# Performance work log

Measured on AMD Instinct MI355X. Metric: run time of the kernel, lower is better.

Reference implementation:

```python
import jax, jax.numpy as jnp
import numpy as np


def _l2_normalize(x, eps=1e-12):
    # matches torch F.normalize(p=2): x / max(||x||, eps)
    n = jnp.linalg.norm(x, axis=-1, keepdims=True)
    return x / jnp.maximum(n, eps)


def _linear_sum_assignment(cost):
    """Jonker-Volgenant shortest augmenting path (same optimum as scipy
    linear_sum_assignment) for a square cost matrix. Returns col4row:
    col4row[r] = column assigned to row r (minimization)."""
    n = cost.shape[0]
    INF = np.inf
    u = np.zeros(n + 1)
    v = np.zeros(n + 1)
    p = np.zeros(n + 1, dtype=np.int64)   # p[j] = row (1-based) assigned to col j
    way = np.zeros(n + 1, dtype=np.int64)
    for i in range(1, n + 1):
        p[0] = i
        j0 = 0
        minv = np.full(n + 1, INF)
        used = np.zeros(n + 1, dtype=bool)
        while True:
            used[j0] = True
            i0 = p[j0]
            cur = cost[i0 - 1] - u[i0] - v[1:]          # reduced costs of row i0
            free = ~used[1:]
            upd = free & (cur < minv[1:])
            idx = np.nonzero(upd)[0]
            minv[idx + 1] = cur[idx]
            way[idx + 1] = j0
            freeidx = np.nonzero(free)[0]
            jrel = freeidx[np.argmin(minv[freeidx + 1])]
            delta = minv[jrel + 1]
            u[p[used]] += delta
            v[used] -= delta
            minv[~used] -= delta
            j0 = jrel + 1
            if p[j0] == 0:
                break
        while j0:
            j1 = way[j0]
            p[j0] = p[j1]
            j0 = j1
    col4row = np.empty(n, dtype=np.int64)
    col4row[p[1:] - 1] = np.arange(n)
    return col4row


def setup_inputs() -> dict:
    key = jax.random.key(0)
    k1, k2 = jax.random.split(key)
    B, N, D = 128, 256, 64
    inputs = jax.random.normal(k1, (B, N, D), dtype=jnp.float32)
    targets = jax.random.normal(k2, (B, N, D), dtype=jnp.float32)
    return {"inputs": inputs, "targets": targets}


def reference(inputs, targets):
    ip = _l2_normalize(inputs)                     # [B, N, D]
    tg = _l2_normalize(targets)                    # [B, N, D]
    cos = jnp.einsum('bad,bcd->bac', ip, tg)       # [B, N, N]
    self_cos = jnp.einsum('bad,bcd->bac', ip, ip)  # [B, N, N]
    # strip the diagonal: tril(-1)[:, :-1] + triu(1)[:, 1:] -> [B, N, N-1]
    self_off = jnp.tril(self_cos, k=-1)[:, :, :-1] + jnp.triu(self_cos, k=1)[:, :, 1:]
    # Hungarian assignment on host (non-differentiable, as in the torch code)
    cost = np.asarray(jax.lax.stop_gradient(-cos))
    tgt = jnp.asarray(np.stack([_linear_sum_assignment(cost[b]) for b in range(cost.shape[0])]))  # [B, N]
    logits = jnp.concatenate([cos, self_off], axis=-1)        # [B, N, 2N-1]
    logp = jax.nn.log_softmax(logits, axis=-1)
    nll = -jnp.take_along_axis(logp, tgt[..., None], axis=-1)[..., 0]  # [B, N]
    # per-sample cross_entropy is mean over N; batch_loss / B -> global mean
    return jnp.mean(nll)
```

## Files before the change

### kernel.cpp

```cpp
#include <hip/hip_runtime.h>
#include <hip/hip_fp16.h>
#include <math.h>

#define BB 128
#define NN 256
#define DD 64
constexpr int NROWS = BB * NN;

__global__ __launch_bounds__(256) void norm_kernel(const float* __restrict__ inp,
                                                   const float* __restrict__ tgin,
                                                   float* __restrict__ ipn,
                                                   float* __restrict__ tgn) {
  int wid = threadIdx.x >> 6;
  int lane = threadIdx.x & 63;
  int row = blockIdx.x * 4 + wid;
  const float* src;
  float* dst;
  int r = row;
  if (row < NROWS) { src = inp; dst = ipn; }
  else { src = tgin; dst = tgn; r = row - NROWS; }
  float x = src[(size_t)r * DD + lane];
  float s = x * x;
  #pragma unroll
  for (int off = 32; off; off >>= 1) s += __shfl_xor(s, off);
  float nrm = sqrtf(s);
  float scale = 1.0f / fmaxf(nrm, 1e-12f);
  dst[(size_t)r * DD + lane] = x * scale;
}

__global__ __launch_bounds__(256) void gemm_kernel(const float* __restrict__ ipn,
                                                   const float* __restrict__ tgn,
                                                   float* __restrict__ cosm,
                                                   float* __restrict__ selfm) {
  __shared__ float As[64 * 64];
  __shared__ float Bs[64 * 64];
  int b = blockIdx.y;
  int ti = (blockIdx.x >> 2) * 64;
  int tj = (blockIdx.x & 3) * 64;
  const float* A = ipn + (size_t)b * NN * DD + (size_t)ti * DD;
  const float* Bm = (blockIdx.z ? ipn : tgn) + (size_t)b * NN * DD + (size_t)tj * DD;
  float* Out = (blockIdx.z ? selfm : cosm) + (size_t)b * NN * NN;
  int t = threadIdx.x;
  #pragma unroll
  for (int i = 0; i < 4; ++i) {
    int f4 = t + 256 * i;
    int row = f4 >> 4;
    int k0 = (f4 & 15) << 2;
    float4 a = reinterpret_cast<const float4*>(A)[f4];
    float4 v = reinterpret_cast<const float4*>(Bm)[f4];
    As[(k0 + 0) * 64 + row] = a.x; As[(k0 + 1) * 64 + row] = a.y;
    As[(k0 + 2) * 64 + row] = a.z; As[(k0 + 3) * 64 + row] = a.w;
    Bs[(k0 + 0) * 64 + row] = v.x; Bs[(k0 + 1) * 64 + row] = v.y;
    Bs[(k0 + 2) * 64 + row] = v.z; Bs[(k0 + 3) * 64 + row] = v.w;
  }
  __syncthreads();
  int tx = t & 15, ty = t >> 4;
  float acc[4][4] = {};
  #pragma unroll 8
  for (int k = 0; k < 64; ++k) {
    float4 av = *reinterpret_cast<const float4*>(&As[k * 64 + ty * 4]);
    float4 bv = *reinterpret_cast<const float4*>(&Bs[k * 64 + tx * 4]);
    float ar[4] = {av.x, av.y, av.z, av.w};
    float br[4] = {bv.x, bv.y, bv.z, bv.w};
    #pragma unroll
    for (int r = 0; r < 4; ++r)
      #pragma unroll
      for (int c = 0; c < 4; ++c)
        acc[r][c] = fmaf(ar[r], br[c], acc[r][c]);
  }
  #pragma unroll
  for (int r = 0; r < 4; ++r) {
    float4 o = {acc[r][0], acc[r][1], acc[r][2], acc[r][3]};
    *reinterpret_cast<float4*>(&Out[(size_t)(ti + ty * 4 + r) * NN + tj + tx * 4]) = o;
  }
}

__device__ __forceinline__ int sel4i(const int a[4], int q) {
  int r = a[0];
  if (q == 1) r = a[1];
  else if (q == 2) r = a[2];
  else if (q == 3) r = a[3];
  return r;
}
__device__ __forceinline__ void set4i(int a[4], int q, int v) {
  if (q == 0) a[0] = v;
  else if (q == 1) a[1] = v;
  else if (q == 2) a[2] = v;
  else a[3] = v;
}
__device__ __forceinline__ int readlane_i(int x, int l) {
  return __builtin_amdgcn_readlane(x, l);
}
__device__ __forceinline__ float readlane_f(float x, int l) {
  return __builtin_bit_cast(float, __builtin_amdgcn_readlane(__builtin_bit_cast(int, x), l));
}
__device__ __forceinline__ float wave_min_f32(float x) {
  float t;
  #define DPP_STEP(ctrl)                                                            \
    t = __builtin_bit_cast(float, __builtin_amdgcn_update_dpp(                      \
            __builtin_bit_cast(int, x), __builtin_bit_cast(int, x), ctrl, 0xF, 0xF, \
            false));                                                                \
    x = fminf(x, t);
  DPP_STEP(0x111)
  DPP_STEP(0x112)
  DPP_STEP(0x114)
  DPP_STEP(0x118)
  DPP_STEP(0x142)
  DPP_STEP(0x143)
  #undef DPP_STEP
  return x;
}

__global__ __launch_bounds__(64) void hungarian_kernel(const float* __restrict__ cosm,
                                                       int* __restrict__ tgt) {
  const int b = blockIdx.x;
  const float* __restrict__ C = cosm + (size_t)b * NN * NN;
  __shared__ __half Cs[NN * NN];
  __shared__ float u_lds[NN];
  const int lane = threadIdx.x;
  const float FINF = INFINITY;

  const float4* Cf4 = reinterpret_cast<const float4*>(C);
  #pragma unroll 4
  for (int it = 0; it < NN * NN / 4 / 64; ++it) {
    float4 f = Cf4[it * 64 + lane];
    __half2 h01 = __floats2half2_rn(f.x, f.y);
    __half2 h23 = __floats2half2_rn(f.z, f.w);
    __half2* dst = reinterpret_cast<__half2*>(&Cs[(it * 64 + lane) * 4]);
    dst[0] = h01;
    dst[1] = h23;
  }
  #pragma unroll
  for (int q = 0; q < 4; ++q) u_lds[lane * 4 + q] = 0.f;

  float v[4] = {0.f, 0.f, 0.f, 0.f};
  int p[4] = {0, 0, 0, 0};

  for (int i = 1; i <= NN; ++i) {
    float minv[4] = {FINF, FINF, FINF, FINF};
    int way[4] = {-2, -2, -2, -2};
    int usedm = 0;
    float Delta = 0.f;
    int j0 = -1;
    float u_i0 = 0.f;
    int row = i - 1;
    uint2 raw = *reinterpret_cast<const uint2*>(&Cs[(size_t)row * NN + lane * 4]);
    int jf;

    while (true) {
      __half2 h01 = __builtin_bit_cast(__half2, raw.x);
      __half2 h23 = __builtin_bit_cast(__half2, raw.y);
      float2 f01 = __half22float2(h01);
      float2 f23 = __half22float2(h23);
      float cc[4] = {f01.x, f01.y, f23.x, f23.y};
      float t0 = Delta - u_i0;
      float cand[4];
      #pragma unroll
      for (int q = 0; q < 4; ++q) {
        float dnew = t0 - cc[q] - v[q];
        bool freeq = !((usedm >> q) & 1);
        if (freeq && dnew < minv[q]) { minv[q] = dnew; way[q] = j0; }
        cand[q] = freeq ? minv[q] : FINF;
      }
      float bv = cand[0];
      int bc = lane * 4;
      #pragma unroll
      for (int q = 1; q < 4; ++q)
        if (cand[q] < bv) { bv = cand[q]; bc = lane * 4 + q; }
      float m = wave_min_f32(bv);
      float K = readlane_f(m, 63);
      unsigned long long mask = __ballot(bv == K);
      int l0 = __ffsll(mask) - 1;
      int j1 = readlane_i(bc, l0);
      Delta = K;
      int pnext = readlane_i(sel4i(p, j1 & 3), j1 >> 2);
      if (pnext == 0) { jf = j1; break; }
      if (lane == (j1 >> 2)) usedm |= 1 << (j1 & 3);
      j0 = j1;
      row = pnext - 1;
      raw = *reinterpret_cast<const uint2*>(&Cs[(size_t)row * NN + lane * 4]);
      u_i0 = u_lds[row];
    }

    #pragma unroll
    for (int q = 0; q < 4; ++q) {
      if ((usedm >> q) & 1) {
        float dd = Delta - minv[q];
        v[q] -= dd;
        u_lds[p[q] - 1] += dd;
      }
    }
    if (lane == 0) u_lds[i - 1] = Delta;

    int j = jf;
    while (true) {
      int w = readlane_i(sel4i(way, j & 3), j >> 2);
      int newv;
      if (w < 0) newv = i;
      else newv = readlane_i(sel4i(p, w & 3), w >> 2);
      if (lane == (j >> 2)) set4i(p, j & 3, newv);
      if (w < 0) break;
      j = w;
    }
  }
  #pragma unroll
  for (int q = 0; q < 4; ++q)
    tgt[(size_t)b * NN + (p[q] - 1)] = lane * 4 + q;
}

__global__ __launch_bounds__(256) void nll_kernel(const float* __restrict__ cosm,
                                                  const float* __restrict__ selfm,
                                                  const int* __restrict__ tgt,
                                                  float* __restrict__ nll) {
  int lane = threadIdx.x & 63, wid = threadIdx.x >> 6;
  int row = blockIdx.x * 4 + wid;
  int r = row & (NN - 1);
  const float* crow = cosm + (size_t)row * NN;
  const float* srow = selfm + (size_t)row * NN;
  float xc[4], xs[4];
  float m = -INFINITY;
  #pragma unroll
  for (int q = 0; q < 4; ++q) {
    int j = lane + 64 * q;
    xc[q] = crow[j];
    xs[q] = (j == r) ? -INFINITY : srow[j];
    m = fmaxf(m, fmaxf(xc[q], xs[q]));
  }
  #pragma unroll
  for (int off = 32; off; off >>= 1) m = fmaxf(m, __shfl_xor(m, off));
  float s = 0.f;
  #pragma unroll
  for (int q = 0; q < 4; ++q) {
    s += expf(xc[q] - m);
    s += (xs[q] == -INFINITY) ? 0.f : expf(xs[q] - m);
  }
  #pragma unroll
  for (int off = 32; off; off >>= 1) s += __shfl_xor(s, off);
  if (lane == 0) {
    float lse = m + logf(s);
    nll[row] = lse - crow[tgt[row]];
  }
}

__global__ __launch_bounds__(256) void reduce_kernel(const float* __restrict__ nll,
                                                     float* __restrict__ out) {
  __shared__ float sm[256];
  int t = threadIdx.x;
  float s = 0.f;
  for (int i = t; i < NROWS; i += 256) s += nll[i];
  sm[t] = s;
  __syncthreads();
  for (int st = 128; st; st >>= 1) {
    if (t < st) sm[t] += sm[t + st];
    __syncthreads();
  }
  if (t == 0) out[0] = sm[0] / (float)NROWS;
}

extern "C" void kernel_launch(void* const* d_in, const int* in_sizes, int n_in,
                              void* d_out, int out_size, void* d_ws, size_t ws_size,
                              hipStream_t stream) {
  const float* inputs = (const float*)d_in[0];
  const float* targets = (const float*)d_in[1];
  float* ws = (float*)d_ws;
  float* ipn = ws;
  float* tgn = ipn + (size_t)BB * NN * DD;
  float* cosm = tgn + (size_t)BB * NN * DD;
  float* selfm = cosm + (size_t)BB * NN * NN;
  int* tgt = (int*)(selfm + (size_t)BB * NN * NN);
  float* nll = (float*)(tgt + BB * NN);

  norm_kernel<<<2 * NROWS / 4, 256, 0, stream>>>(inputs, targets, ipn, tgn);
  gemm_kernel<<<dim3(16, BB, 2), 256, 0, stream>>>(ipn, tgn, cosm, selfm);
  hungarian_kernel<<<BB, 64, 0, stream>>>(cosm, tgt);
  nll_kernel<<<NROWS / 4, 256, 0, stream>>>(cosm, selfm, tgt, nll);
  reduce_kernel<<<1, 256, 0, stream>>>(nll, (float*)d_out);
}
```

Measured before the change: 1.303 ms.

## Switch Hungarian solver to packed integer keys with fused column index

The Hungarian kernel now quantizes the cost into 16-bit fixed-point integers in LDS and runs the shortest-augmenting-path loop in integer arithmetic. The reduced distance and the column index are packed into one 32-bit key, so a single unsigned wave-min gives both the minimum and its argmin. This drops the ballot/ffs/readlane argmin sequence and the half-to-float conversions from the serial inner loop. The next row load is also issued earlier in the loop. In exchange the costs are quantized to about 1/32768, and ties between columns are broken by lowest index. The change assumes the packed key never overflows, so assignments on near-tied costs may differ from the float version.

```diff
diff --git a/kernel.cpp b/kernel.cpp
--- a/kernel.cpp
+++ b/kernel.cpp
@@ -1,5 +1,4 @@
 #include <hip/hip_runtime.h>
-#include <hip/hip_fp16.h>
 #include <math.h>
 
 #define BB 128
@@ -91,16 +90,12 @@
 __device__ __forceinline__ int readlane_i(int x, int l) {
   return __builtin_amdgcn_readlane(x, l);
 }
-__device__ __forceinline__ float readlane_f(float x, int l) {
-  return __builtin_bit_cast(float, __builtin_amdgcn_readlane(__builtin_bit_cast(int, x), l));
-}
-__device__ __forceinline__ float wave_min_f32(float x) {
-  float t;
-  #define DPP_STEP(ctrl)                                                            \
-    t = __builtin_bit_cast(float, __builtin_amdgcn_update_dpp(                      \
-            __builtin_bit_cast(int, x), __builtin_bit_cast(int, x), ctrl, 0xF, 0xF, \
-            false));                                                                \
-    x = fminf(x, t);
+__device__ __forceinline__ unsigned wave_min_u32(unsigned x) {
+  unsigned t;
+  #define DPP_STEP(ctrl)                                                        \
+    t = (unsigned)__builtin_amdgcn_update_dpp((int)x, (int)x, ctrl, 0xF, 0xF,   \
+                                              false);                           \
+    x = (t < x) ? t : x;
   DPP_STEP(0x111)
   DPP_STEP(0x112)
   DPP_STEP(0x114)
@@ -115,78 +110,83 @@
                                                        int* __restrict__ tgt) {
   const int b = blockIdx.x;
   const float* __restrict__ C = cosm + (size_t)b * NN * NN;
-  __shared__ __half Cs[NN * NN];
-  __shared__ float u_lds[NN];
+  __shared__ unsigned short Cs[NN * NN];
+  __shared__ int u_lds[NN];
   const int lane = threadIdx.x;
-  const float FINF = INFINITY;
+  const int col0 = lane * 4;
 
   const float4* Cf4 = reinterpret_cast<const float4*>(C);
   #pragma unroll 4
   for (int it = 0; it < NN * NN / 4 / 64; ++it) {
     float4 f = Cf4[it * 64 + lane];
-    __half2 h01 = __floats2half2_rn(f.x, f.y);
-    __half2 h23 = __floats2half2_rn(f.z, f.w);
-    __half2* dst = reinterpret_cast<__half2*>(&Cs[(it * 64 + lane) * 4]);
-    dst[0] = h01;
-    dst[1] = h23;
-  }
-  #pragma unroll
-  for (int q = 0; q < 4; ++q) u_lds[lane * 4 + q] = 0.f;
-
-  float v[4] = {0.f, 0.f, 0.f, 0.f};
+    unsigned u0 = __float2uint_rn(fmaxf(32768.f - f.x * 32768.f, 0.f));
+    unsigned u1 = __float2uint_rn(fmaxf(32768.f - f.y * 32768.f, 0.f));
+    unsigned u2 = __float2uint_rn(fmaxf(32768.f - f.z * 32768.f, 0.f));
+    unsigned u3 = __float2uint_rn(fmaxf(32768.f - f.w * 32768.f, 0.f));
+    u0 = u0 > 65535u ? 65535u : u0;
+    u1 = u1 > 65535u ? 65535u : u1;
+    u2 = u2 > 65535u ? 65535u : u2;
+    u3 = u3 > 65535u ? 65535u : u3;
+    uint2 packed;
+    packed.x = u0 | (u1 << 16);
+    packed.y = u2 | (u3 << 16);
+    *reinterpret_cast<uint2*>(&Cs[(it * 64 + lane) * 4]) = packed;
+  }
+  #pragma unroll
+  for (int q = 0; q < 4; ++q) u_lds[col0 + q] = 0;
+
+  int vv[4];
+  #pragma unroll
+  for (int q = 0; q < 4; ++q) vv[q] = col0 + q;
   int p[4] = {0, 0, 0, 0};
 
   for (int i = 1; i <= NN; ++i) {
-    float minv[4] = {FINF, FINF, FINF, FINF};
-    int way[4] = {-2, -2, -2, -2};
+    unsigned key[4] = {0xFFFFFFFFu, 0xFFFFFFFFu, 0xFFFFFFFFu, 0xFFFFFFFFu};
+    int way[4] = {-1, -1, -1, -1};
     int usedm = 0;
-    float Delta = 0.f;
+    int Delta = 0;
     int j0 = -1;
-    float u_i0 = 0.f;
+    int u_i0 = 0;
     int row = i - 1;
-    uint2 raw = *reinterpret_cast<const uint2*>(&Cs[(size_t)row * NN + lane * 4]);
+    uint2 raw = *reinterpret_cast<const uint2*>(&Cs[(size_t)row * NN + col0]);
     int jf;
 
     while (true) {
-      __half2 h01 = __builtin_bit_cast(__half2, raw.x);
-      __half2 h23 = __builtin_bit_cast(__half2, raw.y);
-      float2 f01 = __half22float2(h01);
-      float2 f23 = __half22float2(h23);
-      float cc[4] = {f01.x, f01.y, f23.x, f23.y};
-      float t0 = Delta - u_i0;
-      float cand[4];
+      int t0s8 = (Delta - u_i0) << 8;
+      int cs[4];
+      cs[0] = (int)((raw.x & 0xFFFFu) << 8);
+      cs[1] = (int)((raw.x >> 8) & 0x00FFFF00u);
+      cs[2] = (int)((raw.y & 0xFFFFu) << 8);
+      cs[3] = (int)((raw.y >> 8) & 0x00FFFF00u);
       #pragma unroll
       for (int q = 0; q < 4; ++q) {
-        float dnew = t0 - cc[q] - v[q];
-        bool freeq = !((usedm >> q) & 1);
-        if (freeq && dnew < minv[q]) { minv[q] = dnew; way[q] = j0; }
-        cand[q] = freeq ? minv[q] : FINF;
+        unsigned nk = (unsigned)(t0s8 + cs[q] + vv[q]);
+        if (nk < key[q]) { key[q] = nk; way[q] = j0; }
       }
-      float bv = cand[0];
-      int bc = lane * 4;
-      #pragma unroll
-      for (int q = 1; q < 4; ++q)
-        if (cand[q] < bv) { bv = cand[q]; bc = lane * 4 + q; }
-      float m = wave_min_f32(bv);
-      float K = readlane_f(m, 63);
-      unsigned long long mask = __ballot(bv == K);
-      int l0 = __ffsll(mask) - 1;
-      int j1 = readlane_i(bc, l0);
-      Delta = K;
+      unsigned c0 = (usedm & 1) ? 0xFFFFFFFFu : key[0];
+      unsigned c1 = (usedm & 2) ? 0xFFFFFFFFu : key[1];
+      unsigned c2 = (usedm & 4) ? 0xFFFFFFFFu : key[2];
+      unsigned c3 = (usedm & 8) ? 0xFFFFFFFFu : key[3];
+      unsigned loc = c0 < c1 ? c0 : c1;
+      unsigned l2 = c2 < c3 ? c2 : c3;
+      loc = loc < l2 ? loc : l2;
+      unsigned K = (unsigned)readlane_i((int)wave_min_u32(loc), 63);
+      int j1 = (int)(K & 0xFFu);
+      Delta = (int)(K >> 8);
       int pnext = readlane_i(sel4i(p, j1 & 3), j1 >> 2);
       if (pnext == 0) { jf = j1; break; }
+      row = pnext - 1;
+      raw = *reinterpret_cast<const uint2*>(&Cs[(size_t)row * NN + col0]);
+      u_i0 = u_lds[row];
       if (lane == (j1 >> 2)) usedm |= 1 << (j1 & 3);
       j0 = j1;
-      row = pnext - 1;
-      raw = *reinterpret_cast<const uint2*>(&Cs[(size_t)row * NN + lane * 4]);
-      u_i0 = u_lds[row];
     }
 
     #pragma unroll
     for (int q = 0; q < 4; ++q) {
       if ((usedm >> q) & 1) {
-        float dd = Delta - minv[q];
-        v[q] -= dd;
+        int dd = Delta - (int)(key[q] >> 8);
+        vv[q] += dd << 8;
         u_lds[p[q] - 1] += dd;
       }
     }
@@ -205,7 +205,7 @@
   }
   #pragma unroll
   for (int q = 0; q < 4; ++q)
-    tgt[(size_t)b * NN + (p[q] - 1)] = lane * 4 + q;
+    tgt[(size_t)b * NN + (p[q] - 1)] = col0 + q;
 }
 
 __global__ __launch_bounds__(256) void nll_kernel(const float* __restrict__ cosm,
```

Result: no change. 1.283 ms (-1.5%).
